# Kernel tuning notes

Hardware: AMD Instinct MI355X
Metric: run time of the kernel (lower is better)

The kernel has to match this reference:

```python
import jax, jax.numpy as jnp
import numpy as np

BN_EPS = 1e-5
MAX_NODES = 35  # sigmoid()*30+5 floored -> in [5, 34], strict bound 35


def _bn_eval(x, gamma, beta, rm, rv):
    # BatchNorm1d in eval mode with running statistics
    return (x - rm) * (gamma / jnp.sqrt(rv + BN_EPS)) + beta


def setup_inputs() -> dict:
    key = jax.random.key(0)
    ks = jax.random.split(key, 32)
    B, LD, E, ND = 131072, 32, 64, 11

    def lin(k, fan_in, fan_out):
        k1, k2 = jax.random.split(k)
        lim = 1.0 / np.sqrt(fan_in)
        w = jax.random.uniform(k1, (fan_in, fan_out), jnp.float32, -lim, lim)
        b = jax.random.uniform(k2, (fan_out,), jnp.float32, -lim, lim)
        return w, b

    lin_w, lin_b = lin(ks[0], LD + 1, E)
    nn1_w, nn1_b = lin(ks[1], E, E)
    nn2_w, nn2_b = lin(ks[2], E, 1)
    nd1_w, nd1_b = lin(ks[3], E, E)
    nd2_w, nd2_b = lin(ks[4], E, ND)
    pd1_w, pd1_b = lin(ks[5], E, E)
    pd2_w, pd2_b = lin(ks[6], E, 3)

    def bn_params(k):
        k1, k2, k3, k4 = jax.random.split(k, 4)
        gamma = 1.0 + 0.1 * jax.random.normal(k1, (E,), jnp.float32)
        beta = 0.1 * jax.random.normal(k2, (E,), jnp.float32)
        rm = 0.1 * jax.random.normal(k3, (E,), jnp.float32)
        rv = jax.random.uniform(k4, (E,), jnp.float32, 0.5, 1.5)
        return gamma, beta, rm, rv

    nd_gamma, nd_beta, nd_rm, nd_rv = bn_params(ks[7])
    pd_gamma, pd_beta, pd_rm, pd_rv = bn_params(ks[8])

    return dict(
        z=jax.random.normal(ks[9], (B, LD), jnp.float32),
        target_property=jax.random.normal(ks[10], (B,), jnp.float32),
        batch_size=B,
        lin_w=lin_w, lin_b=lin_b,
        nn1_w=nn1_w, nn1_b=nn1_b, nn2_w=nn2_w, nn2_b=nn2_b,
        nd1_w=nd1_w, nd1_b=nd1_b, nd_gamma=nd_gamma, nd_beta=nd_beta,
        nd_rm=nd_rm, nd_rv=nd_rv, nd2_w=nd2_w, nd2_b=nd2_b,
        pd1_w=pd1_w, pd1_b=pd1_b, pd_gamma=pd_gamma, pd_beta=pd_beta,
        pd_rm=pd_rm, pd_rv=pd_rv, pd2_w=pd2_w, pd2_b=pd2_b,
        node_scale=jnp.float32(4.5), node_shift=jnp.float32(4.5),
        pos_scale=jnp.float32(5.0), pos_shift=jnp.float32(0.0),
    )


def reference(z, target_property, batch_size,
              lin_w, lin_b,
              nn1_w, nn1_b, nn2_w, nn2_b,
              nd1_w, nd1_b, nd_gamma, nd_beta, nd_rm, nd_rv, nd2_w, nd2_b,
              pd1_w, pd1_b, pd_gamma, pd_beta, pd_rm, pd_rv, pd2_w, pd2_b,
              node_scale, node_shift, pos_scale, pos_shift):
    tp = target_property.reshape(-1, 1)
    h = jnp.concatenate([z, tp], axis=1) @ lin_w + lin_b  # [B, E]

    nn_logit = jax.nn.relu(h @ nn1_w + nn1_b) @ nn2_w + nn2_b  # [B, 1]
    num_nodes = (jax.nn.sigmoid(nn_logit) * 30.0 + 5.0).astype(jnp.int32)[:, 0]  # [B]

    # Expanded rows per graph are identical copies of h[i], so decode once per
    # graph (BN in eval mode) and repeat -> same math as per-graph expand+MLP.
    nf = _bn_eval(jax.nn.relu(h @ nd1_w + nd1_b), nd_gamma, nd_beta, nd_rm, nd_rv) @ nd2_w + nd2_b
    nf = nf * node_scale + node_shift  # [B, 11]
    pos = _bn_eval(jax.nn.relu(h @ pd1_w + pd1_b), pd_gamma, pd_beta, pd_rm, pd_rv) @ pd2_w + pd2_b
    pos = pos * pos_scale + pos_shift  # [B, 3]

    total = batch_size * MAX_NODES  # static padded bound on ragged concat length
    node_features = jnp.repeat(nf, num_nodes, axis=0, total_repeat_length=total)
    positions = jnp.repeat(pos, num_nodes, axis=0, total_repeat_length=total)
    return node_features, positions, num_nodes
```

## Files before the change

kernel.cpp:

```cpp
#include <hip/hip_runtime.h>
#include <math.h>

typedef unsigned int u32;
typedef unsigned short u16;
typedef unsigned long long u64;
typedef __attribute__((ext_vector_type(8))) short short8v;
typedef __attribute__((ext_vector_type(4))) float f32x4;

#define NDF 11
#define MAXN 35
#define RS 72
#define NFP 12
#define PSP 4

__device__ __forceinline__ u16 f2bf(float x) {
    u32 b = __float_as_uint(x);
    u32 r = (b + 0x7fffu + ((b >> 16) & 1u)) >> 16;
    return (u16)r;
}
__device__ __forceinline__ float bf2f(u16 h) {
    return __uint_as_float(((u32)h) << 16);
}
__device__ __forceinline__ void splitbf(float x, u16& hi, u16& lo) {
    hi = f2bf(x);
    lo = f2bf(x - bf2f(hi));
}

__global__ void k_prep(const float* __restrict__ lin_w,
                       const float* __restrict__ nn1_w, const float* __restrict__ nn2_w,
                       const float* __restrict__ nd1_w, const float* __restrict__ nd2_w,
                       const float* __restrict__ pd1_w, const float* __restrict__ pd2_w,
                       const float* __restrict__ nd_g, const float* __restrict__ nd_be,
                       const float* __restrict__ nd_rm, const float* __restrict__ nd_rv,
                       const float* __restrict__ pd_g, const float* __restrict__ pd_be,
                       const float* __restrict__ pd_rm, const float* __restrict__ pd_rv,
                       u16* __restrict__ lint, u16* __restrict__ w1t3,
                       u16* __restrict__ w2t3, float* __restrict__ bnc)
{
    const int t0 = blockIdx.x * 256 + threadIdx.x;
    if (t0 < 64) {
        const float sc = nd_g[t0] / sqrtf(nd_rv[t0] + 1e-5f);
        bnc[t0]       = sc;
        bnc[64 + t0]  = nd_be[t0] - nd_rm[t0] * sc;
        const float sp = pd_g[t0] / sqrtf(pd_rv[t0] + 1e-5f);
        bnc[128 + t0] = sp;
        bnc[192 + t0] = pd_be[t0] - pd_rm[t0] * sp;
    }
    for (int i = t0; i < 64*RS; i += 4096) {
        const int n = i / RS, k = i % RS;
        const float v = (k < 33) ? lin_w[k*64 + n] : 0.f;
        u16 h, l; splitbf(v, h, l);
        lint[i] = h; lint[64*RS + i] = l;
    }
    for (int b = 0; b < 3; b++) {
        const float* M = (b == 0) ? nn1_w : (b == 1) ? nd1_w : pd1_w;
        u16* dst = w1t3 + (size_t)b * 2 * 64 * RS;
        for (int i = t0; i < 64*RS; i += 4096) {
            const int o = i / RS, k = i % RS;
            const float v = (k < 64) ? M[k*64 + o] : 0.f;
            u16 h, l; splitbf(v, h, l);
            dst[i] = h; dst[64*RS + i] = l;
        }
        u16* d2 = w2t3 + (size_t)b * 2 * 16 * RS;
        for (int i = t0; i < 16*RS; i += 4096) {
            const int n = i / RS, k = i % RS;
            float v = 0.f;
            if (k < 64) {
                if (b == 0)      { if (n == 14)           v = nn2_w[k]; }
                else if (b == 1) { if (n < 11)            v = nd2_w[k*11 + n]; }
                else             { if (n >= 11 && n < 14) v = pd2_w[k*3 + (n-11)]; }
            }
            u16 h, l; splitbf(v, h, l);
            d2[i] = h; d2[16*RS + i] = l;
        }
    }
}

__global__ __launch_bounds__(256)
void k_mfma(const float* __restrict__ z, const float* __restrict__ tpr,
            const float* __restrict__ lin_w, const float* __restrict__ lin_b,
            const u16* __restrict__ lint, const u16* __restrict__ w1t3,
            const u16* __restrict__ w2t3,
            const float* __restrict__ nn1_b, const float* __restrict__ nd1_b,
            const float* __restrict__ pd1_b,
            const float* __restrict__ nn2_b, const float* __restrict__ nd2_b,
            const float* __restrict__ pd2_b,
            const float* __restrict__ bnc,
            const float* __restrict__ nsc, const float* __restrict__ nsh,
            const float* __restrict__ psc, const float* __restrict__ psh,
            float* __restrict__ nf_g, float* __restrict__ pos_g,
            int* __restrict__ nn_int, float* __restrict__ out_nn,
            u32* __restrict__ fmask, int B)
{
    __shared__ __align__(16) u16 sXT[4][2*16*RS];
    __shared__ __align__(16) u16 sH[4][2*16*RS];

    const int t    = threadIdx.x;
    const int lane = t & 63;
    const int w    = t >> 6;
    u16* mX = sXT[w];
    u16* mH = sH[w];

    const int W = blockIdx.x * 4 + w;

    auto gfrag = [&](const u16* base, int row0, int ks) -> short8v {
        const uint4 v = *(const uint4*)(base + (row0 + (lane & 15))*RS + ks*32 + ((lane >> 4) * 8));
        return __builtin_bit_cast(short8v, v);
    };
    short8v fLin[4], fW[3][4][2], fH2[3][2];
    #pragma unroll
    for (int nt = 0; nt < 4; nt++)
        fLin[nt] = gfrag(lint, nt*16, 0);
    #pragma unroll
    for (int b = 0; b < 3; b++)
        #pragma unroll
        for (int nt = 0; nt < 4; nt++)
            #pragma unroll
            for (int ks = 0; ks < 2; ks++)
                fW[b][nt][ks] = gfrag(w1t3 + (size_t)b*2*64*RS, nt*16, ks);
    #pragma unroll
    for (int b = 0; b < 3; b++)
        #pragma unroll
        for (int ks = 0; ks < 2; ks++)
            fH2[b][ks] = gfrag(w2t3 + (size_t)b*2*16*RS, 0, ks);

    const int col = lane & 15;
    float bLin[4], lin32c[4], bB1[3][4], bSc[2][4], bBi[2][4];
    #pragma unroll
    for (int nt = 0; nt < 4; nt++) {
        const int c = nt*16 + col;
        bLin[nt]    = lin_b[c];
        lin32c[nt]  = lin_w[32*64 + c];
        bB1[0][nt]  = nn1_b[c];
        bB1[1][nt]  = nd1_b[c];
        bB1[2][nt]  = pd1_b[c];
        bSc[0][nt]  = bnc[c];        bBi[0][nt] = bnc[64 + c];
        bSc[1][nt]  = bnc[128 + c];  bBi[1][nt] = bnc[192 + c];
    }
    const float epb = (col < 11) ? nd2_b[col] : (col < 14) ? pd2_b[col - 11] : 0.f;
    const float nn2b = nn2_b[0];
    const float a_ns = nsc[0], a_nh = nsh[0], a_ps = psc[0], a_ph = psh[0];

    auto ldfrag = [&](const u16* base, int ks) -> short8v {
        const uint4 v = *(const uint4*)(base + (lane & 15)*RS + ks*32 + ((lane >> 4) * 8));
        return __builtin_bit_cast(short8v, v);
    };

    u32 wavebits = 0;

    #pragma unroll 1
    for (int c = 0; c < 2; c++) {
        const int gb = (W*2 + c) * 16;
        if (gb >= B) break;

        {
            const float4* zb = (const float4*)(z + (size_t)gb * 32);
            const float4 v0 = zb[(lane >> 2)*8 + (lane & 3)*2];
            const float4 v1 = zb[(lane >> 2)*8 + (lane & 3)*2 + 1];
            const float xv[8] = {v0.x, v0.y, v0.z, v0.w, v1.x, v1.y, v1.z, v1.w};
            u32 pkh[4], pkl[4];
            #pragma unroll
            for (int q = 0; q < 4; q++) {
                u16 h0, l0, h1, l1;
                splitbf(xv[2*q], h0, l0);
                splitbf(xv[2*q+1], h1, l1);
                pkh[q] = (u32)h0 | ((u32)h1 << 16);
                pkl[q] = (u32)l0 | ((u32)l1 << 16);
            }
            *(uint4*)(mX + (lane >> 2)*RS + (lane & 3)*8) = *(uint4*)pkh;
            *(uint4*)(mX + 16*RS + (lane >> 2)*RS + (lane & 3)*8) = *(uint4*)pkl;
        }

        const float4 tq = *(const float4*)(tpr + gb + (lane >> 4)*4);
        const float tpf[4] = {tq.x, tq.y, tq.z, tq.w};

        const short8v a0h = ldfrag(mX, 0);
        const short8v a0l = ldfrag(mX + 16*RS, 0);
        #pragma unroll
        for (int nt = 0; nt < 4; nt++) {
            const short8v bl0 = gfrag(lint + 64*RS, nt*16, 0);
            f32x4 acc = {0.f, 0.f, 0.f, 0.f};
            acc = __builtin_amdgcn_mfma_f32_16x16x32_bf16(a0h, fLin[nt], acc, 0, 0, 0);
            acc = __builtin_amdgcn_mfma_f32_16x16x32_bf16(a0h, bl0, acc, 0, 0, 0);
            acc = __builtin_amdgcn_mfma_f32_16x16x32_bf16(a0l, fLin[nt], acc, 0, 0, 0);
            const float bias = bLin[nt];
            const float l32 = lin32c[nt];
            #pragma unroll
            for (int r = 0; r < 4; r++) {
                const int row = (lane >> 4)*4 + r;
                const float hv = fmaf(tpf[r], l32, acc[r] + bias);
                u16 hh, hl; splitbf(hv, hh, hl);
                mH[row*RS + nt*16 + col] = hh;
                mH[16*RS + row*RS + nt*16 + col] = hl;
            }
        }

        u16* mT = mX;
        const short8v h0h = ldfrag(mH, 0);
        const short8v h1h = ldfrag(mH, 1);
        f32x4 acc2 = {0.f, 0.f, 0.f, 0.f};

        {
            const short8v h0l = ldfrag(mH + 16*RS, 0);
            const short8v h1l = ldfrag(mH + 16*RS, 1);
            const u16* wlo = w1t3 + 64*RS;
            #pragma unroll
            for (int nt = 0; nt < 4; nt++) {
                const short8v wl0 = gfrag(wlo, nt*16, 0);
                const short8v wl1 = gfrag(wlo, nt*16, 1);
                f32x4 acc = {0.f, 0.f, 0.f, 0.f};
                acc = __builtin_amdgcn_mfma_f32_16x16x32_bf16(h0h, fW[0][nt][0], acc, 0, 0, 0);
                acc = __builtin_amdgcn_mfma_f32_16x16x32_bf16(h1h, fW[0][nt][1], acc, 0, 0, 0);
                acc = __builtin_amdgcn_mfma_f32_16x16x32_bf16(h0h, wl0, acc, 0, 0, 0);
                acc = __builtin_amdgcn_mfma_f32_16x16x32_bf16(h1h, wl1, acc, 0, 0, 0);
                acc = __builtin_amdgcn_mfma_f32_16x16x32_bf16(h0l, fW[0][nt][0], acc, 0, 0, 0);
                acc = __builtin_amdgcn_mfma_f32_16x16x32_bf16(h1l, fW[0][nt][1], acc, 0, 0, 0);
                const float bb = bB1[0][nt];
                #pragma unroll
                for (int r = 0; r < 4; r++) {
                    const int row = (lane >> 4)*4 + r;
                    float rv = acc[r] + bb;
                    rv = rv > 0.f ? rv : 0.f;
                    u16 th, tl; splitbf(rv, th, tl);
                    mT[row*RS + nt*16 + col] = th;
                    mT[16*RS + row*RS + nt*16 + col] = tl;
                }
            }
            const short8v t0h = ldfrag(mT, 0);
            const short8v t1h = ldfrag(mT, 1);
            const short8v t0l = ldfrag(mT + 16*RS, 0);
            const short8v t1l = ldfrag(mT + 16*RS, 1);
            const short8v g2l0 = gfrag(w2t3 + 16*RS, 0, 0);
            const short8v g2l1 = gfrag(w2t3 + 16*RS, 0, 1);
            acc2 = __builtin_amdgcn_mfma_f32_16x16x32_bf16(t0h, fH2[0][0], acc2, 0, 0, 0);
            acc2 = __builtin_amdgcn_mfma_f32_16x16x32_bf16(t1h, fH2[0][1], acc2, 0, 0, 0);
            acc2 = __builtin_amdgcn_mfma_f32_16x16x32_bf16(t0h, g2l0, acc2, 0, 0, 0);
            acc2 = __builtin_amdgcn_mfma_f32_16x16x32_bf16(t1h, g2l1, acc2, 0, 0, 0);
            acc2 = __builtin_amdgcn_mfma_f32_16x16x32_bf16(t0l, fH2[0][0], acc2, 0, 0, 0);
            acc2 = __builtin_amdgcn_mfma_f32_16x16x32_bf16(t1l, fH2[0][1], acc2, 0, 0, 0);
        }

        #pragma unroll
        for (int b = 1; b < 3; b++) {
            #pragma unroll
            for (int nt = 0; nt < 4; nt++) {
                f32x4 acc = {0.f, 0.f, 0.f, 0.f};
                acc = __builtin_amdgcn_mfma_f32_16x16x32_bf16(h0h, fW[b][nt][0], acc, 0, 0, 0);
                acc = __builtin_amdgcn_mfma_f32_16x16x32_bf16(h1h, fW[b][nt][1], acc, 0, 0, 0);
                const float bb = bB1[b][nt];
                const float sc = bSc[b-1][nt];
                const float bi = bBi[b-1][nt];
                #pragma unroll
                for (int r = 0; r < 4; r++) {
                    const int row = (lane >> 4)*4 + r;
                    float rv = acc[r] + bb;
                    rv = rv > 0.f ? rv : 0.f;
                    mT[row*RS + nt*16 + col] = f2bf(fmaf(rv, sc, bi));
                }
            }
            const short8v t0 = ldfrag(mT, 0);
            const short8v t1 = ldfrag(mT, 1);
            acc2 = __builtin_amdgcn_mfma_f32_16x16x32_bf16(t0, fH2[b][0], acc2, 0, 0, 0);
            acc2 = __builtin_amdgcn_mfma_f32_16x16x32_bf16(t1, fH2[b][1], acc2, 0, 0, 0);
        }

        u32 chunkbits = 0;
        #pragma unroll
        for (int r = 0; r < 4; r++) {
            const int g = gb + (lane >> 4)*4 + r;
            const float v = acc2[r];
            bool fl = false;
            if (col < 11) {
                nf_g[(size_t)g*NFP + col] = fmaf(v + epb, a_ns, a_nh);
            } else if (col < 14) {
                pos_g[(size_t)g*PSP + (col - 11)] = fmaf(v + epb, a_ps, a_ph);
            } else if (col == 14) {
                const float logit = v + nn2b;
                const float arg = fmaf(1.f / (1.f + expf(-logit)), 30.f, 5.f);
                int n;
                if (arg < 5.03f) {
                    n = 5;
                } else if (arg >= 34.97f) {
                    if (logit >= 38.f)      n = 35;
                    else { n = 34; fl = (logit > 37.f); }
                } else {
                    n = (int)arg;
                    fl = fabsf(arg - rintf(arg)) < 0.03f;
                }
                nn_int[g] = n;
                out_nn[g] = (float)n;
            }
            const u64 m = __ballot(fl);
            chunkbits |= (u32)(((m >> 14) & 1ull) << r)
                       | (u32)(((m >> 30) & 1ull) << (4 + r))
                       | (u32)(((m >> 46) & 1ull) << (8 + r))
                       | (u32)(((m >> 62) & 1ull) << (12 + r));
        }
        wavebits |= chunkbits << (16 * c);
    }

    if (lane == 0) fmask[W] = wavebits;
    (void)B;
}

__global__ __launch_bounds__(256)
void k_fixscan(const float* __restrict__ z, const float* __restrict__ tpr,
               const float* __restrict__ lin_w, const float* __restrict__ lin_b,
               const float* __restrict__ nn1_w, const float* __restrict__ nn1_b,
               const float* __restrict__ nn2_w, const float* __restrict__ nn2_b,
               const u32* __restrict__ fmask, int* __restrict__ nn_int,
               float* __restrict__ out_nn,
               int* __restrict__ part, int* __restrict__ bsum)
{
    __shared__ __align__(16) double hb[4][64];
    __shared__ int s_n[256];
    __shared__ int ws[4];

    const int t = threadIdx.x;
    const int lane = t & 63;
    const int w = t >> 6;
    const int g0 = blockIdx.x * 256;

    s_n[t] = nn_int[g0 + t];

    {
        const u32 m0 = fmask[blockIdx.x*8 + w*2];
        const u32 m1 = fmask[blockIdx.x*8 + w*2 + 1];
        u64 mask = (u64)m0 | ((u64)m1 << 32);
        const double b2 = (double)nn2_b[0];

        while (mask) {
            const int bpos = __ffsll(mask) - 1;
            mask &= mask - 1;
            const int g = g0 + w*64 + bpos;

            double h0 = (double)lin_b[lane], h1 = 0.0, h2 = 0.0, h3 = 0.0;
            for (int j = 0; j < 32; j += 4) {
                h0 = fma((double)z[(size_t)g*32 + j],     (double)lin_w[j*64 + lane],     h0);
                h1 = fma((double)z[(size_t)g*32 + j + 1], (double)lin_w[(j+1)*64 + lane], h1);
                h2 = fma((double)z[(size_t)g*32 + j + 2], (double)lin_w[(j+2)*64 + lane], h2);
                h3 = fma((double)z[(size_t)g*32 + j + 3], (double)lin_w[(j+3)*64 + lane], h3);
            }
            h0 = fma((double)tpr[g], (double)lin_w[32*64 + lane], h0);
            hb[w][lane] = (h0 + h1) + (h2 + h3);

            const double2* hp = (const double2*)hb[w];
            double a0 = (double)nn1_b[lane], a1 = 0.0, a2 = 0.0, a3 = 0.0;
            for (int m = 0; m < 16; m++) {
                const double2 p = hp[2*m];
                const double2 q = hp[2*m + 1];
                a0 = fma(p.x, (double)nn1_w[(4*m+0)*64 + lane], a0);
                a1 = fma(p.y, (double)nn1_w[(4*m+1)*64 + lane], a1);
                a2 = fma(q.x, (double)nn1_w[(4*m+2)*64 + lane], a2);
                a3 = fma(q.y, (double)nn1_w[(4*m+3)*64 + lane], a3);
            }
            const double a = (a0 + a1) + (a2 + a3);
            double v = (a > 0.0) ? a * (double)nn2_w[lane] : 0.0;
            for (int d = 32; d > 0; d >>= 1) v += __shfl_xor(v, d);
            const double logit = v + b2;

            if (lane == 0) {
                const double sg = 1.0 / (1.0 + exp(-logit));
                const int n = (int)(sg * 30.0 + 5.0);
                s_n[w*64 + bpos] = n;
                nn_int[g] = n;
                out_nn[g] = (float)n;
            }
        }
    }
    __syncthreads();

    int v = s_n[t];
    #pragma unroll
    for (int d = 1; d < 64; d <<= 1) {
        const int u = __shfl_up(v, d);
        if (lane >= d) v += u;
    }
    if (lane == 63) ws[w] = v;
    __syncthreads();
    int add = 0;
    #pragma unroll
    for (int q = 0; q < 3; q++) if (q < w) add += ws[q];
    v += add;
    part[g0 + t] = v;
    if (t == 255) bsum[blockIdx.x] = v;
}

__global__ __launch_bounds__(256)
void k_expand(const int* __restrict__ part, const int* __restrict__ bsum,
              const float* __restrict__ nf_g, const float* __restrict__ pos_g,
              float* __restrict__ out, int B, int T, int nb)
{
    __shared__ __align__(16) float s_nf[512*NDF];
    __shared__ __align__(16) float s_ps[512*3];
    __shared__ int s_boff[513];
    __shared__ int ws2[4];
    const int t = threadIdx.x;
    const int lane = t & 63;
    const int wid = t >> 6;

    {
        const int v0 = bsum[2*t];
        const int v1 = bsum[2*t + 1];
        const int s = v0 + v1;
        int sc = s;
        #pragma unroll
        for (int d = 1; d < 64; d <<= 1) {
            const int u = __shfl_up(sc, d);
            if (lane >= d) sc += u;
        }
        if (lane == 63) ws2[wid] = sc;
        __syncthreads();
        int add = 0;
        #pragma unroll
        for (int q = 0; q < 3; q++) if (q < wid) add += ws2[q];
        sc += add;
        const int exc = sc - s;
        s_boff[2*t]     = exc;
        s_boff[2*t + 1] = exc + v0;
        if (t == 255) s_boff[512] = sc;
    }
    __syncthreads();

    const int r0 = blockIdx.x * 512 + 2*t;

    int blo = 0, bhi = nb - 1;
    while (blo < bhi) {
        const int m = (blo + bhi + 1) >> 1;
        if (s_boff[m] <= r0) blo = m; else bhi = m - 1;
    }
    const int bi = blo;
    const int lr = r0 - s_boff[bi];
    int lo = 0, hi2 = 256;
    while (lo < hi2) {
        const int m = (lo + hi2) >> 1;
        if (part[bi*256 + m] <= lr) lo = m + 1; else hi2 = m;
    }
    int i0 = bi*256 + lo;
    i0 = (i0 < B) ? i0 : B - 1;
    const int Ci0 = s_boff[i0 >> 8] + part[i0];
    const int i1 = ((r0 + 1) >= Ci0 && i0 < B - 1) ? i0 + 1 : i0;

    {
        const float4* n0 = (const float4*)(nf_g + (size_t)i0*NFP);
        const float4* n1 = (const float4*)(nf_g + (size_t)i1*NFP);
        const float4 a0 = n0[0], a1 = n0[1], a2 = n0[2];
        const float4 b0 = n1[0], b1 = n1[1], b2 = n1[2];
        float* d0 = s_nf + (2*t)*NDF;
        d0[0] = a0.x; d0[1] = a0.y; d0[2] = a0.z; d0[3] = a0.w;
        d0[4] = a1.x; d0[5] = a1.y; d0[6] = a1.z; d0[7] = a1.w;
        d0[8] = a2.x; d0[9] = a2.y; d0[10] = a2.z;
        float* d1 = s_nf + (2*t + 1)*NDF;
        d1[0] = b0.x; d1[1] = b0.y; d1[2] = b0.z; d1[3] = b0.w;
        d1[4] = b1.x; d1[5] = b1.y; d1[6] = b1.z; d1[7] = b1.w;
        d1[8] = b2.x; d1[9] = b2.y; d1[10] = b2.z;

        const float4 p0 = *(const float4*)(pos_g + (size_t)i0*PSP);
        const float4 p1 = *(const float4*)(pos_g + (size_t)i1*PSP);
        s_ps[(2*t)*3 + 0] = p0.x; s_ps[(2*t)*3 + 1] = p0.y; s_ps[(2*t)*3 + 2] = p0.z;
        s_ps[(2*t + 1)*3 + 0] = p1.x; s_ps[(2*t + 1)*3 + 1] = p1.y; s_ps[(2*t + 1)*3 + 2] = p1.z;
    }
    __syncthreads();

    float4* onf = (float4*)(out + (size_t)blockIdx.x * 512 * NDF);
    const float4* snf = (const float4*)s_nf;
    #pragma unroll
    for (int q = 0; q < 6; q++) {
        const int idx = q*256 + t;
        if (idx < 512*NDF/4) onf[idx] = snf[idx];
    }
    float4* ops = (float4*)(out + (size_t)T*NDF + (size_t)blockIdx.x * 512 * 3);
    const float4* sps = (const float4*)s_ps;
    #pragma unroll
    for (int q = 0; q < 2; q++) {
        const int idx = q*256 + t;
        if (idx < 384) ops[idx] = sps[idx];
    }
}

extern "C" void kernel_launch(void* const* d_in, const int* in_sizes, int n_in,
                              void* d_out, int out_size, void* d_ws, size_t ws_size,
                              hipStream_t stream)
{
    const float* z     = (const float*)d_in[0];
    const float* tpr   = (const float*)d_in[1];
    const int    B     = in_sizes[1];
    const int    T     = B * MAXN;

    const float* lin_w = (const float*)d_in[3];
    const float* lin_b = (const float*)d_in[4];
    const float* nn1_w = (const float*)d_in[5];
    const float* nn1_b = (const float*)d_in[6];
    const float* nn2_w = (const float*)d_in[7];
    const float* nn2_b = (const float*)d_in[8];
    const float* nd1_w = (const float*)d_in[9];
    const float* nd1_b = (const float*)d_in[10];
    const float* nd_g  = (const float*)d_in[11];
    const float* nd_be = (const float*)d_in[12];
    const float* nd_rm = (const float*)d_in[13];
    const float* nd_rv = (const float*)d_in[14];
    const float* nd2_w = (const float*)d_in[15];
    const float* nd2_b = (const float*)d_in[16];
    const float* pd1_w = (const float*)d_in[17];
    const float* pd1_b = (const float*)d_in[18];
    const float* pd_g  = (const float*)d_in[19];
    const float* pd_be = (const float*)d_in[20];
    const float* pd_rm = (const float*)d_in[21];
    const float* pd_rv = (const float*)d_in[22];
    const float* pd2_w = (const float*)d_in[23];
    const float* pd2_b = (const float*)d_in[24];
    const float* nsc   = (const float*)d_in[25];
    const float* nsh   = (const float*)d_in[26];
    const float* psc   = (const float*)d_in[27];
    const float* psh   = (const float*)d_in[28];

    float* out = (float*)d_out;

    char* wsp = (char*)d_ws;
    size_t off = 0;
    auto take = [&](size_t bytes) { void* p = wsp + off; off = (off + bytes + 255) & ~(size_t)255; return p; };

    u16*   lint  = (u16*)take(2*64*RS*sizeof(u16));
    u16*   w1t3  = (u16*)take(3*2*64*RS*sizeof(u16));
    u16*   w2t3  = (u16*)take(3*2*16*RS*sizeof(u16));
    float* bnc   = (float*)take(256*sizeof(float));
    u32*   fmask = (u32*)take((size_t)(B/32)*sizeof(u32));
    float* nf_g  = (float*)take((size_t)B*NFP*sizeof(float));
    float* pos_g = (float*)take((size_t)B*PSP*sizeof(float));
    int*   nn_i  = (int*)take((size_t)B*sizeof(int));
    int*   part  = (int*)take((size_t)B*sizeof(int));
    int*   bsum  = (int*)take(4096*sizeof(int));

    const int nb = B / 256;

    k_prep<<<16, 256, 0, stream>>>(lin_w, nn1_w, nn2_w, nd1_w, nd2_w, pd1_w, pd2_w,
                                   nd_g, nd_be, nd_rm, nd_rv,
                                   pd_g, pd_be, pd_rm, pd_rv,
                                   lint, w1t3, w2t3, bnc);

    k_mfma<<<B/128, 256, 0, stream>>>(z, tpr, lin_w, lin_b, lint, w1t3, w2t3,
                                      nn1_b, nd1_b, pd1_b, nn2_b, nd2_b, pd2_b,
                                      bnc, nsc, nsh, psc, psh,
                                      nf_g, pos_g, nn_i, out + (size_t)T*14,
                                      fmask, B);

    k_fixscan<<<nb, 256, 0, stream>>>(z, tpr, lin_w, lin_b, nn1_w, nn1_b,
                                      nn2_w, nn2_b, fmask, nn_i,
                                      out + (size_t)T*14, part, bsum);

    k_expand<<<T/512, 256, 0, stream>>>(part, bsum, nf_g, pos_g, out, B, T, nb);

    (void)n_in; (void)out_size; (void)ws_size;
}
```

Before: 135.4 us.

## Fuse fp64 borderline fixup into MFMA kernel and widen expand blocks

```diff
diff --git a/kernel.cpp b/kernel.cpp
--- a/kernel.cpp
+++ b/kernel.cpp
@@ -79,6 +79,7 @@
 __global__ __launch_bounds__(256)
 void k_mfma(const float* __restrict__ z, const float* __restrict__ tpr,
             const float* __restrict__ lin_w, const float* __restrict__ lin_b,
+            const float* __restrict__ nn1_w, const float* __restrict__ nn2_w,
             const u16* __restrict__ lint, const u16* __restrict__ w1t3,
             const u16* __restrict__ w2t3,
             const float* __restrict__ nn1_b, const float* __restrict__ nd1_b,
@@ -89,8 +90,7 @@
             const float* __restrict__ nsc, const float* __restrict__ nsh,
             const float* __restrict__ psc, const float* __restrict__ psh,
             float* __restrict__ nf_g, float* __restrict__ pos_g,
-            int* __restrict__ nn_int, float* __restrict__ out_nn,
-            u32* __restrict__ fmask, int B)
+            int* __restrict__ nn_int, float* __restrict__ out_nn, int B)
 {
     __shared__ __align__(16) u16 sXT[4][2*16*RS];
     __shared__ __align__(16) u16 sH[4][2*16*RS];
@@ -287,8 +287,7 @@
                     n = (int)arg;
                     fl = fabsf(arg - rintf(arg)) < 0.03f;
                 }
-                nn_int[g] = n;
-                out_nn[g] = (float)n;
+                if (!fl) { nn_int[g] = n; out_nn[g] = (float)n; }
             }
             const u64 m = __ballot(fl);
             chunkbits |= (u32)(((m >> 14) & 1ull) << r)
@@ -299,40 +298,14 @@
         wavebits |= chunkbits << (16 * c);
     }
 
-    if (lane == 0) fmask[W] = wavebits;
-    (void)B;
-}
-
-__global__ __launch_bounds__(256)
-void k_fixscan(const float* __restrict__ z, const float* __restrict__ tpr,
-               const float* __restrict__ lin_w, const float* __restrict__ lin_b,
-               const float* __restrict__ nn1_w, const float* __restrict__ nn1_b,
-               const float* __restrict__ nn2_w, const float* __restrict__ nn2_b,
-               const u32* __restrict__ fmask, int* __restrict__ nn_int,
-               float* __restrict__ out_nn,
-               int* __restrict__ part, int* __restrict__ bsum)
-{
-    __shared__ __align__(16) double hb[4][64];
-    __shared__ int s_n[256];
-    __shared__ int ws[4];
-
-    const int t = threadIdx.x;
-    const int lane = t & 63;
-    const int w = t >> 6;
-    const int g0 = blockIdx.x * 256;
-
-    s_n[t] = nn_int[g0 + t];
-
     {
-        const u32 m0 = fmask[blockIdx.x*8 + w*2];
-        const u32 m1 = fmask[blockIdx.x*8 + w*2 + 1];
-        u64 mask = (u64)m0 | ((u64)m1 << 32);
+        double* hb = (double*)mH;
         const double b2 = (double)nn2_b[0];
-
+        u32 mask = wavebits;
         while (mask) {
-            const int bpos = __ffsll(mask) - 1;
+            const int bpos = __ffs(mask) - 1;
             mask &= mask - 1;
-            const int g = g0 + w*64 + bpos;
+            const int g = W*32 + bpos;
 
             double h0 = (double)lin_b[lane], h1 = 0.0, h2 = 0.0, h3 = 0.0;
             for (int j = 0; j < 32; j += 4) {
@@ -342,9 +315,9 @@
                 h3 = fma((double)z[(size_t)g*32 + j + 3], (double)lin_w[(j+3)*64 + lane], h3);
             }
             h0 = fma((double)tpr[g], (double)lin_w[32*64 + lane], h0);
-            hb[w][lane] = (h0 + h1) + (h2 + h3);
-
-            const double2* hp = (const double2*)hb[w];
+            hb[lane] = (h0 + h1) + (h2 + h3);
+
+            const double2* hp = (const double2*)hb;
             double a0 = (double)nn1_b[lane], a1 = 0.0, a2 = 0.0, a3 = 0.0;
             for (int m = 0; m < 16; m++) {
                 const double2 p = hp[2*m];
@@ -362,27 +335,35 @@
             if (lane == 0) {
                 const double sg = 1.0 / (1.0 + exp(-logit));
                 const int n = (int)(sg * 30.0 + 5.0);
-                s_n[w*64 + bpos] = n;
                 nn_int[g] = n;
                 out_nn[g] = (float)n;
             }
         }
     }
-    __syncthreads();
-
-    int v = s_n[t];
+    (void)B;
+}
+
+__global__ __launch_bounds__(256)
+void k_scan1(const int* __restrict__ a, int* __restrict__ part, int* __restrict__ bsum)
+{
+    const int t = threadIdx.x;
+    const int lane = t & 63;
+    const int wid = t >> 6;
+    const int g = blockIdx.x * 256 + t;
+    int v = a[g];
     #pragma unroll
     for (int d = 1; d < 64; d <<= 1) {
         const int u = __shfl_up(v, d);
         if (lane >= d) v += u;
     }
-    if (lane == 63) ws[w] = v;
+    __shared__ int ws[4];
+    if (lane == 63) ws[wid] = v;
     __syncthreads();
     int add = 0;
     #pragma unroll
-    for (int q = 0; q < 3; q++) if (q < w) add += ws[q];
+    for (int q = 0; q < 3; q++) if (q < wid) add += ws[q];
     v += add;
-    part[g0 + t] = v;
+    part[g] = v;
     if (t == 255) bsum[blockIdx.x] = v;
 }
 
@@ -391,8 +372,8 @@
               const float* __restrict__ nf_g, const float* __restrict__ pos_g,
               float* __restrict__ out, int B, int T, int nb)
 {
-    __shared__ __align__(16) float s_nf[512*NDF];
-    __shared__ __align__(16) float s_ps[512*3];
+    __shared__ __align__(16) float s_nf[1024*NDF];
+    __shared__ __align__(16) float s_ps[1024*3];
     __shared__ int s_boff[513];
     __shared__ int ws2[4];
     const int t = threadIdx.x;
@@ -422,7 +403,7 @@
     }
     __syncthreads();
 
-    const int r0 = blockIdx.x * 512 + 2*t;
+    const int r0 = blockIdx.x * 1024 + 4*t;
 
     int blo = 0, bhi = nb - 1;
     while (blo < bhi) {
@@ -439,43 +420,42 @@
     int i0 = bi*256 + lo;
     i0 = (i0 < B) ? i0 : B - 1;
     const int Ci0 = s_boff[i0 >> 8] + part[i0];
-    const int i1 = ((r0 + 1) >= Ci0 && i0 < B - 1) ? i0 + 1 : i0;
-
-    {
-        const float4* n0 = (const float4*)(nf_g + (size_t)i0*NFP);
-        const float4* n1 = (const float4*)(nf_g + (size_t)i1*NFP);
-        const float4 a0 = n0[0], a1 = n0[1], a2 = n0[2];
-        const float4 b0 = n1[0], b1 = n1[1], b2 = n1[2];
-        float* d0 = s_nf + (2*t)*NDF;
-        d0[0] = a0.x; d0[1] = a0.y; d0[2] = a0.z; d0[3] = a0.w;
-        d0[4] = a1.x; d0[5] = a1.y; d0[6] = a1.z; d0[7] = a1.w;
-        d0[8] = a2.x; d0[9] = a2.y; d0[10] = a2.z;
-        float* d1 = s_nf + (2*t + 1)*NDF;
-        d1[0] = b0.x; d1[1] = b0.y; d1[2] = b0.z; d1[3] = b0.w;
-        d1[4] = b1.x; d1[5] = b1.y; d1[6] = b1.z; d1[7] = b1.w;
-        d1[8] = b2.x; d1[9] = b2.y; d1[10] = b2.z;
-
-        const float4 p0 = *(const float4*)(pos_g + (size_t)i0*PSP);
-        const float4 p1 = *(const float4*)(pos_g + (size_t)i1*PSP);
-        s_ps[(2*t)*3 + 0] = p0.x; s_ps[(2*t)*3 + 1] = p0.y; s_ps[(2*t)*3 + 2] = p0.z;
-        s_ps[(2*t + 1)*3 + 0] = p1.x; s_ps[(2*t + 1)*3 + 1] = p1.y; s_ps[(2*t + 1)*3 + 2] = p1.z;
+    const bool canadv = (i0 < B - 1);
+    const int i1 = canadv ? i0 + 1 : i0;
+
+    const float4* n0 = (const float4*)(nf_g + (size_t)i0*NFP);
+    const float4* n1 = (const float4*)(nf_g + (size_t)i1*NFP);
+    const float4 a0 = n0[0], a1 = n0[1], a2 = n0[2];
+    const float4 b0 = n1[0], b1 = n1[1], b2 = n1[2];
+    const float4 p0 = *(const float4*)(pos_g + (size_t)i0*PSP);
+    const float4 p1 = *(const float4*)(pos_g + (size_t)i1*PSP);
+
+    #pragma unroll
+    for (int rr = 0; rr < 4; rr++) {
+        const bool adv = canadv && ((r0 + rr) >= Ci0);
+        float* d = s_nf + (4*t + rr)*NDF;
+        const float4 c0 = adv ? b0 : a0;
+        const float4 c1 = adv ? b1 : a1;
+        const float4 c2 = adv ? b2 : a2;
+        d[0] = c0.x; d[1] = c0.y; d[2] = c0.z; d[3] = c0.w;
+        d[4] = c1.x; d[5] = c1.y; d[6] = c1.z; d[7] = c1.w;
+        d[8] = c2.x; d[9] = c2.y; d[10] = c2.z;
+        const float4 pp = adv ? p1 : p0;
+        float* e = s_ps + (4*t + rr)*3;
+        e[0] = pp.x; e[1] = pp.y; e[2] = pp.z;
     }
     __syncthreads();
 
-    float4* onf = (float4*)(out + (size_t)blockIdx.x * 512 * NDF);
-    const float4* snf = (const float4*)s_nf;
-    #pragma unroll
-    for (int q = 0; q < 6; q++) {
-        const int idx = q*256 + t;
-        if (idx < 512*NDF/4) onf[idx] = snf[idx];
-    }
-    float4* ops = (float4*)(out + (size_t)T*NDF + (size_t)blockIdx.x * 512 * 3);
-    const float4* sps = (const float4*)s_ps;
-    #pragma unroll
-    for (int q = 0; q < 2; q++) {
-        const int idx = q*256 + t;
-        if (idx < 384) ops[idx] = sps[idx];
-    }
+    f32x4* onf = (f32x4*)(out + (size_t)blockIdx.x * 1024 * NDF);
+    const f32x4* snf = (const f32x4*)s_nf;
+    #pragma unroll
+    for (int q = 0; q < 11; q++)
+        __builtin_nontemporal_store(snf[q*256 + t], onf + q*256 + t);
+    f32x4* ops = (f32x4*)(out + (size_t)T*NDF + (size_t)blockIdx.x * 1024 * 3);
+    const f32x4* sps = (const f32x4*)s_ps;
+    #pragma unroll
+    for (int q = 0; q < 3; q++)
+        __builtin_nontemporal_store(sps[q*256 + t], ops + q*256 + t);
 }
 
 extern "C" void kernel_launch(void* const* d_in, const int* in_sizes, int n_in,
@@ -524,7 +504,6 @@
     u16*   w1t3  = (u16*)take(3*2*64*RS*sizeof(u16));
     u16*   w2t3  = (u16*)take(3*2*16*RS*sizeof(u16));
     float* bnc   = (float*)take(256*sizeof(float));
-    u32*   fmask = (u32*)take((size_t)(B/32)*sizeof(u32));
     float* nf_g  = (float*)take((size_t)B*NFP*sizeof(float));
     float* pos_g = (float*)take((size_t)B*PSP*sizeof(float));
     int*   nn_i  = (int*)take((size_t)B*sizeof(int));
@@ -538,17 +517,15 @@
                                    pd_g, pd_be, pd_rm, pd_rv,
                                    lint, w1t3, w2t3, bnc);
 
-    k_mfma<<<B/128, 256, 0, stream>>>(z, tpr, lin_w, lin_b, lint, w1t3, w2t3,
+    k_mfma<<<B/128, 256, 0, stream>>>(z, tpr, lin_w, lin_b, nn1_w, nn2_w,
+                                      lint, w1t3, w2t3,
                                       nn1_b, nd1_b, pd1_b, nn2_b, nd2_b, pd2_b,
                                       bnc, nsc, nsh, psc, psh,
-                                      nf_g, pos_g, nn_i, out + (size_t)T*14,
-                                      fmask, B);
-
-    k_fixscan<<<nb, 256, 0, stream>>>(z, tpr, lin_w, lin_b, nn1_w, nn1_b,
-                                      nn2_w, nn2_b, fmask, nn_i,
-                                      out + (size_t)T*14, part, bsum);
-
-    k_expand<<<T/512, 256, 0, stream>>>(part, bsum, nf_g, pos_g, out, B, T, nb);
+                                      nf_g, pos_g, nn_i, out + (size_t)T*14, B);
+
+    k_scan1<<<nb, 256, 0, stream>>>(nn_i, part, bsum);
+
+    k_expand<<<T/1024, 256, 0, stream>>>(part, bsum, nf_g, pos_g, out, B, T, nb);
 
     (void)n_in; (void)out_size; (void)ws_size;
 }
```

Result: slower. 142.0 us (+4.8%).
